# Performance work log

Hardware: AMD Instinct MI355X
Metric: run time of the kernel (lower is better)

The kernel has to match this reference:

```python
import jax, jax.numpy as jnp
import numpy as np
import math

# Model hyperparameters (match init_kwargs)
B, S, E = 8, 1024, 512
NUM_HEADS = 8
NQ = 16        # n_qubits for quantum attention
NQF = 16       # n_qubits_ffn for quantum feed-forward
FFN = 2048
L = 4          # num_layers
EPS = 1e-5


def _sinusoidal_pe(seq_len, embed_dim):
    pos = np.arange(seq_len)[:, None].astype(np.float32)
    div = np.exp(np.arange(0, embed_dim, 2).astype(np.float32) * (-math.log(10000.0) / embed_dim))
    pe = np.zeros((seq_len, embed_dim), dtype=np.float32)
    pe[:, 0::2] = np.sin(pos * div)
    pe[:, 1::2] = np.cos(pos * div)
    return jnp.asarray(pe)


def setup_inputs() -> dict:
    key = jax.random.key(0)
    ks = jax.random.split(key, 12)
    x = jax.random.normal(ks[0], (B, S, E), dtype=jnp.float32)
    pe = _sinusoidal_pe(S, E)
    # per-layer parameters stacked along leading L axis
    theta_attn = jax.random.normal(ks[1], (L, NQ), dtype=jnp.float32) * 0.1   # RY angles (attention circuit)
    theta_ffn = jax.random.normal(ks[2], (L, NQF), dtype=jnp.float32) * 0.1    # RY angles (ffn circuit)
    W_combine = jax.random.normal(ks[3], (L, E, NQ), dtype=jnp.float32) / math.sqrt(NQ)
    W1 = jax.random.normal(ks[4], (L, FFN, NQF), dtype=jnp.float32) / math.sqrt(NQF)
    W2 = jax.random.normal(ks[5], (L, E, FFN), dtype=jnp.float32) / math.sqrt(FFN)
    g1 = jnp.ones((L, E), dtype=jnp.float32)
    b1 = jnp.zeros((L, E), dtype=jnp.float32)
    g2 = jnp.ones((L, E), dtype=jnp.float32)
    b2 = jnp.zeros((L, E), dtype=jnp.float32)
    return {"x": x, "pe": pe, "theta_attn": theta_attn, "theta_ffn": theta_ffn,
            "W_combine": W_combine, "W1": W1, "W2": W2,
            "g1": g1, "b1": b1, "g2": g2, "b2": b2}


def _layer_norm(h, g, b):
    m = jnp.mean(h, axis=-1, keepdims=True)
    v = jnp.var(h, axis=-1, keepdims=True)
    return (h - m) * jax.lax.rsqrt(v + EPS) * g + b


def _quantum_features(h, theta, n_qubits):
    # Each wire: |0> -> RX(x_i) -> RY(theta_i) -> <Z_i> = cos(theta_i) * cos(x_i)
    # Product state => exact closed form; vectorizes the per-token circuit loop.
    return jnp.cos(theta)[None, None, :] * jnp.cos(h[..., :n_qubits])


def reference(x, pe, theta_attn, theta_ffn, W_combine, W1, W2, g1, b1, g2, b2):
    b_, s_, e_ = x.shape
    dk = NQ // NUM_HEADS
    h = x + pe[None, :s_, :]
    for l in range(L):
        qv = _quantum_features(h, theta_attn[l], NQ)                 # [B,S,NQ]
        q = qv.reshape(b_, s_, NUM_HEADS, dk).transpose(0, 2, 1, 3)  # [B,H,S,dk]
        scores = jnp.einsum('bhqd,bhkd->bhqk', q, q) / math.sqrt(dk)
        probs = jax.nn.softmax(scores, axis=-1)
        attn = jnp.einsum('bhqk,bhkd->bhqd', probs, q)               # [B,H,S,dk]
        attn = attn.transpose(0, 2, 1, 3).reshape(b_, s_, NQ)
        attn_out = attn @ W_combine[l].T                             # [B,S,E]
        h = _layer_norm(h + attn_out, g1[l], b1[l])
        # --- quantum feed-forward ---
        qf = _quantum_features(h, theta_ffn[l], NQF)                 # [B,S,NQF]
        ffn_out = jax.nn.relu(qf @ W1[l].T) @ W2[l].T                # [B,S,E]
        h = _layer_norm(h + ffn_out, g2[l], b2[l])
    return h
```

## Files before the change

kernel.cpp:

```cpp
#include <hip/hip_runtime.h>
#include <cstdint>
#include <cstddef>

#define BB 8
#define SS 1024
#define EE 512
#define NQB 16
#define FF 2048

typedef unsigned short u16;
typedef __attribute__((ext_vector_type(8))) short short8;
typedef __attribute__((ext_vector_type(4))) float f32x4;
typedef unsigned int uint_g __attribute__((address_space(1)));
typedef unsigned int uint_l __attribute__((address_space(3)));

#define FLAG_OFF   0
#define H16_OFF    4096
#define QF_OFF     528384
#define W1P_OFF    1052672
#define STATS_OFF  1314816
#define H_OFF      2097152
#define W2P_OFF    18874368

__device__ __forceinline__ float u2f(u16 u){ return __uint_as_float(((unsigned)u)<<16); }
__device__ __forceinline__ u16 f2bf(float x){
  unsigned u = __float_as_uint(x);
  u += 0x7FFF + ((u>>16)&1);
  return (u16)(u>>16);
}
__device__ __forceinline__ float ldg(const void* p,int f,size_t i){
  return f ? ((const float*)p)[i] : u2f(((const u16*)p)[i]);
}
__device__ __forceinline__ float4 ldg4(const void* p,int f,size_t i){
  float4 r;
  if (f){ r = ((const float4*)p)[i>>2]; }
  else { ushort4 v = ((const ushort4*)p)[i>>2];
         r.x=u2f(v.x); r.y=u2f(v.y); r.z=u2f(v.z); r.w=u2f(v.w); }
  return r;
}
__device__ __forceinline__ short8 ldfrag8(const void* p,int f,size_t i){
  short8 r;
  if (f){
    float4 A  = ((const float4*)p)[i>>2];
    float4 Bv = ((const float4*)p)[(i>>2)+1];
    r[0]=(short)f2bf(A.x);  r[1]=(short)f2bf(A.y);  r[2]=(short)f2bf(A.z);  r[3]=(short)f2bf(A.w);
    r[4]=(short)f2bf(Bv.x); r[5]=(short)f2bf(Bv.y); r[6]=(short)f2bf(Bv.z); r[7]=(short)f2bf(Bv.w);
  } else {
    r = *(const short8*)((const u16*)p + i);
  }
  return r;
}
__device__ __forceinline__ void async16(const void* g, void* l){
  __builtin_amdgcn_global_load_lds((const uint_g*)g, (uint_l*)l, 16, 0, 0);
}
__device__ __forceinline__ void tok_stats(const float* st, int tok, float& m, float& rs){
  float S1 = 0.f, S2 = 0.f;
  #pragma unroll
  for (int nb=0; nb<4; ++nb){
    float2 p = *(const float2*)&st[((size_t)tok*4+nb)*2];
    S1 += p.x; S2 += p.y;
  }
  m = S1*(1.f/512.f);
  float var = S2*(1.f/512.f) - m*m;
  rs = rsqrtf(var + 1e-5f);
}

__global__ void detect_k(const u16* __restrict__ x, int* __restrict__ flag){
  __shared__ int cnt;
  if (threadIdx.x==0) cnt=0;
  __syncthreads();
  int c=0;
  for (int i=threadIdx.x;i<4096;i+=256){
    u16 v = x[(size_t)i*2];
    int ex = (v>>7)&0xFF;
    c += (ex>=160) ? 1 : 0;
  }
  atomicAdd(&cnt,c);
  __syncthreads();
  if (threadIdx.x==0) *flag = (cnt>64) ? 1 : 0;
}

__global__ __launch_bounds__(256) void w1pack_k(const void* __restrict__ W1,
    const void* __restrict__ thf, u16* __restrict__ W1p, const int* __restrict__ flag){
  int f = *flag;
  int idx = blockIdx.x*256 + threadIdx.x;
  int l = idx>>12, nt = (idx>>5)&127, lane32 = idx&31;
  int quad = lane32>>4, col = lane32&15;
  short8 v = ldfrag8(W1, f, ((size_t)l*FF + nt*16 + col)*16 + quad*8);
  short8 o;
  #pragma unroll
  for (int j=0;j<8;++j){
    float th = ldg(thf, f, (size_t)l*16 + quad*8 + j);
    o[j] = (short)f2bf(__cosf(th) * u2f((u16)v[j]));
  }
  *(short8*)(W1p + (size_t)idx*8) = o;
}

__global__ __launch_bounds__(256) void w2pack_k(const void* __restrict__ W2,
    u16* __restrict__ W2p, const int* __restrict__ flag){
  int f = *flag;
  int idx = blockIdx.x*256 + threadIdx.x;
  int lane = idx&63, kb = (idx>>6)&63, teg = (idx>>12)&31, l = idx>>17;
  int quad = lane>>4, col = lane&15;
  short8 v = ldfrag8(W2, f, ((size_t)l*EE + teg*16 + col)*FF + kb*32 + quad*8);
  *(short8*)(W2p + (size_t)idx*8) = v;
}

__global__ __launch_bounds__(256) void add_pe_k(const void* __restrict__ x,
    const void* __restrict__ pe, float* __restrict__ hw, const int* __restrict__ flag){
  int f = *flag;
  size_t e = ((size_t)blockIdx.x*256 + threadIdx.x)*4;
  float4 xv = ldg4(x,f,e);
  float4 pv = ldg4(pe,f,e & (size_t)(SS*EE-1));
  float4 o; o.x=xv.x+pv.x; o.y=xv.y+pv.y; o.z=xv.z+pv.z; o.w=xv.w+pv.w;
  *(float4*)&hw[e] = o;
}

__global__ __launch_bounds__(256) void attn_comb_k(float* __restrict__ hw,
    const void* __restrict__ thA, const void* __restrict__ Wc,
    const void* __restrict__ g1v, const void* __restrict__ b1v,
    const void* __restrict__ g2v, const void* __restrict__ b2v,
    const float* __restrict__ st, float* __restrict__ h16,
    float* __restrict__ qf, const int* __restrict__ flag, int lazy, int l){
  __shared__ float SM2[19264];
  float* qq   = SM2;
  float* outC = SM2;
  float* msK  = SM2 + 16640;
  float* AFR  = SM2 + 18688;
  float* MS   = SM2 + 19200;
  float* RS   = SM2 + 19232;
  int f = *flag;
  int tid = threadIdx.x;
  int b = blockIdx.x>>5, grp = blockIdx.x&31;
  size_t bbase = (size_t)b*SS*EE;
  int tok0 = b*SS + grp*32;

  if (lazy){
    #pragma unroll
    for (int t2=0;t2<4;++t2){
      int j = tid*4+t2;
      float m, rs; tok_stats(st, b*SS+j, m, rs);
      msK[j*2]=m; msK[j*2+1]=rs;
    }
  }
  __syncthreads();
  {
    int j0 = tid>>2, d0 = (tid&3)*4;
    float ct[4], gl2[4]={1,1,1,1}, bl2[4]={0,0,0,0};
    #pragma unroll
    for (int d=0;d<4;++d) ct[d] = __cosf(ldg(thA,f,(size_t)l*16+d0+d));
    if (lazy){
      float4 gv = ldg4(g2v,f,(size_t)(l-1)*EE+d0);
      float4 bv = ldg4(b2v,f,(size_t)(l-1)*EE+d0);
      gl2[0]=gv.x; gl2[1]=gv.y; gl2[2]=gv.z; gl2[3]=gv.w;
      bl2[0]=bv.x; bl2[1]=bv.y; bl2[2]=bv.z; bl2[3]=bv.w;
    }
    for (int it=0; it<16; ++it){
      int j = j0 + it*64;
      float4 hv = *(const float4*)&hw[bbase + (size_t)j*EE + d0];
      float vv[4] = {hv.x, hv.y, hv.z, hv.w};
      if (lazy){
        float m = msK[j*2], rs = msK[j*2+1];
        #pragma unroll
        for (int d=0;d<4;++d) vv[d] = fmaf((vv[d]-m)*rs, gl2[d], bl2[d]);
      }
      float4 o;
      o.x = ct[0]*__cosf(vv[0]); o.y = ct[1]*__cosf(vv[1]);
      o.z = ct[2]*__cosf(vv[2]); o.w = ct[3]*__cosf(vv[3]);
      *(float4*)&qq[j*16+d0] = o;
    }
  }
  __syncthreads();
  {
    int r = tid&31, hd = tid>>5;
    int rg = grp*32 + r;
    float a0 = qq[rg*16 + 2*hd], a1 = qq[rg*16 + 2*hd + 1];
    const float sc = 0.70710678118f;
    float a0s = a0*sc, a1s = a1*sc;
    float den=0.f, n0=0.f, n1=0.f;
    for (int j=0;j<SS;++j){
      float2 uv = *(const float2*)&qq[j*16 + 2*hd];
      float e = __expf(fmaf(a1s, uv.y, a0s*uv.x));
      den += e; n0 = fmaf(e, uv.x, n0); n1 = fmaf(e, uv.y, n1);
    }
    float inv = 1.f/den;
    AFR[r*16 + 2*hd] = n0*inv; AFR[r*16 + 2*hd + 1] = n1*inv;
  }
  __syncthreads();
  int e0 = tid*2;
  float wc0[16], wc1[16];
  size_t wb = (size_t)l*EE*16;
  #pragma unroll
  for (int q4=0;q4<4;++q4){
    float4 a = ldg4(Wc,f, wb + (size_t)e0*16     + q4*4);
    float4 bq = ldg4(Wc,f, wb + (size_t)(e0+1)*16 + q4*4);
    wc0[q4*4+0]=a.x; wc0[q4*4+1]=a.y; wc0[q4*4+2]=a.z; wc0[q4*4+3]=a.w;
    wc1[q4*4+0]=bq.x; wc1[q4*4+1]=bq.y; wc1[q4*4+2]=bq.z; wc1[q4*4+3]=bq.w;
  }
  float gl0=1.f,bl0=0.f,gl1=1.f,bl1=0.f;
  if (lazy){
    size_t gb = (size_t)(l-1)*EE;
    gl0 = ldg(g2v,f,gb+e0);   bl0 = ldg(b2v,f,gb+e0);
    gl1 = ldg(g2v,f,gb+e0+1); bl1 = ldg(b2v,f,gb+e0+1);
  }
  for (int t=0; t<32; ++t){
    float2 hr = *(const float2*)&hw[(size_t)(tok0+t)*EE + e0];
    float v0 = hr.x, v1 = hr.y;
    if (lazy){
      float m = msK[(grp*32+t)*2], rs = msK[(grp*32+t)*2+1];
      v0 = fmaf((v0-m)*rs, gl0, bl0);
      v1 = fmaf((v1-m)*rs, gl1, bl1);
    }
    float s0 = v0, s1 = v1;
    #pragma unroll
    for (int q4=0;q4<4;++q4){
      float4 av = *(const float4*)&AFR[t*16 + q4*4];
      s0 = fmaf(av.x, wc0[q4*4+0], fmaf(av.y, wc0[q4*4+1], fmaf(av.z, wc0[q4*4+2], fmaf(av.w, wc0[q4*4+3], s0))));
      s1 = fmaf(av.x, wc1[q4*4+0], fmaf(av.y, wc1[q4*4+1], fmaf(av.z, wc1[q4*4+2], fmaf(av.w, wc1[q4*4+3], s1))));
    }
    outC[t*520 + e0] = s0; outC[t*520 + e0 + 1] = s1;
  }
  __syncthreads();
  {
    int token = tid>>3, prt = tid&7;
    float s=0.f, s2=0.f;
    #pragma unroll 8
    for (int i2=0;i2<64;++i2){
      float vv = outC[token*520 + prt + 8*i2];
      s += vv; s2 = fmaf(vv,vv,s2);
    }
    #pragma unroll
    for (int off=4; off; off>>=1){ s += __shfl_down(s,off,8); s2 += __shfl_down(s2,off,8); }
    if (prt==0){
      float m = s*(1.f/512.f);
      float var = s2*(1.f/512.f) - m*m;
      MS[token] = m; RS[token] = rsqrtf(var+1e-5f);
    }
  }
  __syncthreads();
  for (int u=tid; u<32*128; u+=256){
    int tok = u>>7, c4 = (u&127)*4;
    float4 vv = *(const float4*)&outC[tok*520 + c4];
    float m = MS[tok], rs = RS[tok];
    float4 gv = ldg4(g1v,f,(size_t)l*EE + c4);
    float4 bv = ldg4(b1v,f,(size_t)l*EE + c4);
    float4 o;
    o.x = fmaf((vv.x-m)*rs, gv.x, bv.x);
    o.y = fmaf((vv.y-m)*rs, gv.y, bv.y);
    o.z = fmaf((vv.z-m)*rs, gv.z, bv.z);
    o.w = fmaf((vv.w-m)*rs, gv.w, bv.w);
    if (c4 >= 16){
      *(float4*)&hw[(size_t)(tok0+tok)*EE + c4] = o;
    } else {
      *(float4*)&h16[(size_t)(tok0+tok)*16 + c4] = o;
      float4 qo;
      qo.x=__cosf(o.x); qo.y=__cosf(o.y); qo.z=__cosf(o.z); qo.w=__cosf(o.w);
      *(float4*)&qf[(size_t)(tok0+tok)*16 + c4] = qo;
    }
  }
}

__global__ __launch_bounds__(256) void ffn4_k(float* __restrict__ hw,
    const float* __restrict__ h16, const float* __restrict__ qf,
    const u16* __restrict__ W1p, const void* __restrict__ W2,
    const u16* __restrict__ W2p, float* __restrict__ st,
    const int* __restrict__ flag, int cv, int l){
  __shared__ float SMF[12288];
  u16* W2t = (u16*)SMF;
  u16* HtA = (u16*)SMF + 16384;
  float* outL = SMF;

  int f = *flag;
  int tid = threadIdx.x, w = tid>>6, lane = tid&63;
  int quad = lane>>4, col = lane&15;
  int mb = blockIdx.x, nb = blockIdx.y;
  int tok0 = mb*64;
  int wm = w&1, wn = w>>1;

  short8 a0[4];
  #pragma unroll
  for (int mt=0; mt<4; ++mt){
    short8 z = {0,0,0,0,0,0,0,0};
    if (quad < 2){
      const float* qp = qf + (size_t)(tok0 + mt*16 + col)*16 + quad*8;
      float4 A = *(const float4*)qp, B = *(const float4*)(qp+4);
      z[0]=(short)f2bf(A.x); z[1]=(short)f2bf(A.y); z[2]=(short)f2bf(A.z); z[3]=(short)f2bf(A.w);
      z[4]=(short)f2bf(B.x); z[5]=(short)f2bf(B.y); z[6]=(short)f2bf(B.z); z[7]=(short)f2bf(B.w);
    }
    a0[mt] = z;
  }

  f32x4 acc[2][4];
  #pragma unroll
  for (int i=0;i<2;++i)
    #pragma unroll
    for (int j=0;j<4;++j) acc[i][j] = (f32x4){0.f,0.f,0.f,0.f};
  const f32x4 zc = {0.f,0.f,0.f,0.f};
  size_t w2base = (size_t)l*EE*FF;

  auto stage = [&](int k0, int buf){
    if (cv){
      #pragma unroll
      for (int fi=0; fi<4; ++fi){
        int slot = w*4+fi, te = slot>>1, s = slot&1;
        int kb = (k0>>5) + s;
        const u16* gp = W2p + (((size_t)l*32 + nb*8 + te)*64 + kb)*512 + lane*8;
        async16(gp, &W2t[buf*8192 + slot*512 + lane*8]);
      }
    } else {
      #pragma unroll
      for (int fi=0; fi<4; ++fi){
        int slot = w*4+fi, te = slot>>1, s = slot&1;
        short8 v = ldfrag8(W2, f, w2base + (size_t)(nb*128 + te*16 + col)*FF + k0 + s*32 + quad*8);
        *(short8*)&W2t[buf*8192 + slot*512 + lane*8] = v;
      }
    }
  };
  auto gemm1 = [&](int k0, int buf){
    short8 b1 = {0,0,0,0,0,0,0,0};
    if (quad < 2)
      b1 = *(const short8*)(W1p + (((size_t)l*128 + (k0>>4) + w)*32 + quad*16 + col)*8);
    int kl = w*16 + quad*4;
    int s  = kl>>5, q2 = (kl&31)>>3, j0 = kl&7;
    u16* dst0 = &HtA[buf*4096 + s*512 + (q2*16+col)*8 + j0];
    #pragma unroll
    for (int mt=0; mt<4; ++mt){
      f32x4 hc = __builtin_amdgcn_mfma_f32_16x16x32_bf16(b1, a0[mt], zc, 0,0,0);
      ushort4 pk;
      pk.x = f2bf(fmaxf(hc[0],0.f)); pk.y = f2bf(fmaxf(hc[1],0.f));
      pk.z = f2bf(fmaxf(hc[2],0.f)); pk.w = f2bf(fmaxf(hc[3],0.f));
      *(ushort4*)(dst0 + mt*1024) = pk;
    }
  };

  stage(0, 0); gemm1(0, 0);
  for (int i=0; i<32; ++i){
    __syncthreads();
    int k1 = (i+1)*64;
    if (k1 < FF){ stage(k1, (i+1)&1); gemm1(k1, (i+1)&1); }
    int cb = i&1;
    #pragma unroll
    for (int s=0;s<2;++s){
      short8 A2[2], B2[4];
      A2[0] = *(const short8*)&HtA[cb*4096 + ((wm*2+0)*2+s)*512 + lane*8];
      A2[1] = *(const short8*)&HtA[cb*4096 + ((wm*2+1)*2+s)*512 + lane*8];
      #pragma unroll
      for (int et=0;et<4;++et)
        B2[et] = *(const short8*)&W2t[cb*8192 + ((wn*4+et)*2+s)*512 + lane*8];
      #pragma unroll
      for (int et=0;et<4;++et){
        acc[0][et] = __builtin_amdgcn_mfma_f32_16x16x32_bf16(A2[0], B2[et], acc[0][et], 0,0,0);
        acc[1][et] = __builtin_amdgcn_mfma_f32_16x16x32_bf16(A2[1], B2[et], acc[1][et], 0,0,0);
      }
    }
  }
  __syncthreads();

  #pragma unroll
  for (int mt2=0; mt2<2; ++mt2){
    #pragma unroll
    for (int r=0;r<4;++r){
      int ltok = wm*32 + mt2*16 + quad*4 + r;
      size_t hb = (size_t)(tok0+ltok)*EE + nb*128;
      #pragma unroll
      for (int et=0;et<4;++et){
        int eloc = wn*64 + et*16 + col;
        int eg = nb*128 + eloc;
        float rsd = (eg < 16) ? h16[(size_t)(tok0+ltok)*16 + eg] : hw[hb + eloc];
        outL[ltok*132 + eloc] = acc[mt2][et][r] + rsd;
      }
    }
  }
  __syncthreads();
  {
    int token = tid>>2, prt = tid&3;
    float s=0.f, s2=0.f;
    #pragma unroll 8
    for (int i2=0;i2<32;++i2){
      float vv = outL[token*132 + prt + 4*i2];
      s += vv; s2 = fmaf(vv,vv,s2);
    }
    s += __shfl_down(s,2,4); s2 += __shfl_down(s2,2,4);
    s += __shfl_down(s,1,4); s2 += __shfl_down(s2,1,4);
    if (prt==0){
      float2 o; o.x = s; o.y = s2;
      *(float2*)&st[((size_t)(tok0+token)*4 + nb)*2] = o;
    }
  }
  for (int u=tid; u<64*32; u+=256){
    int tok = u>>5, c4 = (u&31)*4;
    float4 vv = *(const float4*)&outL[tok*132 + c4];
    *(float4*)&hw[(size_t)(tok0+tok)*EE + nb*128 + c4] = vv;
  }
}

__global__ __launch_bounds__(256) void conv2_k(const float* __restrict__ hw,
    const float* __restrict__ st, const void* __restrict__ g2v,
    const void* __restrict__ b2v, void* __restrict__ out,
    const int* __restrict__ flag){
  int f = *flag;
  size_t i = (size_t)blockIdx.x*256 + threadIdx.x;
  int tok = (int)(i>>7), c4 = ((int)i&127)*4;
  float4 v = *(const float4*)&hw[i*4];
  float m, rs; tok_stats(st, tok, m, rs);
  float4 gv = ldg4(g2v,f,(size_t)3*EE + c4);
  float4 bv = ldg4(b2v,f,(size_t)3*EE + c4);
  float4 o;
  o.x = fmaf((v.x-m)*rs, gv.x, bv.x);
  o.y = fmaf((v.y-m)*rs, gv.y, bv.y);
  o.z = fmaf((v.z-m)*rs, gv.z, bv.z);
  o.w = fmaf((v.w-m)*rs, gv.w, bv.w);
  if (f){
    *(float4*)((float*)out + i*4) = o;
  } else {
    ushort4 ob; ob.x=f2bf(o.x); ob.y=f2bf(o.y); ob.z=f2bf(o.z); ob.w=f2bf(o.w);
    *(ushort4*)((u16*)out + i*4) = ob;
  }
}

extern "C" void kernel_launch(void* const* d_in, const int* in_sizes, int n_in,
                              void* d_out, int out_size, void* d_ws, size_t ws_size,
                              hipStream_t stream) {
  (void)in_sizes; (void)n_in; (void)out_size;
  char* ws = (char*)d_ws;
  int*   flag = (int*)(ws + FLAG_OFF);
  float* h16  = (float*)(ws + H16_OFF);
  float* qf   = (float*)(ws + QF_OFF);
  u16*   w1p  = (u16*)(ws + W1P_OFF);
  float* st   = (float*)(ws + STATS_OFF);
  float* hw   = (float*)(ws + H_OFF);
  u16*   w2p  = (u16*)(ws + W2P_OFF);
  int cv = (ws_size >= (size_t)W2P_OFF + ((size_t)8<<20)) ? 1 : 0;

  detect_k<<<1,256,0,stream>>>((const u16*)d_in[0], flag);
  w1pack_k<<<64,256,0,stream>>>(d_in[5], d_in[3], w1p, flag);
  if (cv) w2pack_k<<<2048,256,0,stream>>>(d_in[6], w2p, flag);
  add_pe_k<<<4096,256,0,stream>>>(d_in[0], d_in[1], hw, flag);
  for (int l=0; l<4; ++l){
    int lazy = (l>0) ? 1 : 0;
    attn_comb_k<<<256,256,0,stream>>>(hw, d_in[2], d_in[4], d_in[7], d_in[8],
                                      d_in[9], d_in[10], st, h16, qf,
                                      flag, lazy, l);
    ffn4_k<<<dim3(128,4),256,0,stream>>>(hw, h16, qf, w1p, d_in[6], w2p,
                                         st, flag, cv, l);
  }
  conv2_k<<<4096,256,0,stream>>>(hw, st, d_in[9], d_in[10], d_out, flag);
}
```

Baseline: 448.3 us.

## Split attention key loop across 512 threads and stream W2 directly into registers

The attention/combine kernel now runs 512 threads per block. The softmax key loop is split into two halves whose partial sums are reduced through shared memory, and the q features are stored head-major for float4 reads. The FFN kernel drops LDS staging of W2 and prefetches each wave's W2 fragments straight from global memory into registers. Each wave then owns a 64x32 output tile, which also reduces LDS footprint. This trades LDS traffic and async loads for more register pressure and extra global reads of W2 per block.

```diff
diff --git a/kernel.cpp b/kernel.cpp
--- a/kernel.cpp
+++ b/kernel.cpp
@@ -11,8 +11,6 @@
 typedef unsigned short u16;
 typedef __attribute__((ext_vector_type(8))) short short8;
 typedef __attribute__((ext_vector_type(4))) float f32x4;
-typedef unsigned int uint_g __attribute__((address_space(1)));
-typedef unsigned int uint_l __attribute__((address_space(3)));
 
 #define FLAG_OFF   0
 #define H16_OFF    4096
@@ -50,9 +48,6 @@
   }
   return r;
 }
-__device__ __forceinline__ void async16(const void* g, void* l){
-  __builtin_amdgcn_global_load_lds((const uint_g*)g, (uint_l*)l, 16, 0, 0);
-}
 __device__ __forceinline__ void tok_stats(const float* st, int tok, float& m, float& rs){
   float S1 = 0.f, S2 = 0.f;
   #pragma unroll
@@ -116,19 +111,20 @@
   *(float4*)&hw[e] = o;
 }
 
-__global__ __launch_bounds__(256) void attn_comb_k(float* __restrict__ hw,
+__global__ __launch_bounds__(512) void attn_comb_k(float* __restrict__ hw,
     const void* __restrict__ thA, const void* __restrict__ Wc,
     const void* __restrict__ g1v, const void* __restrict__ b1v,
     const void* __restrict__ g2v, const void* __restrict__ b2v,
     const float* __restrict__ st, float* __restrict__ h16,
     float* __restrict__ qf, const int* __restrict__ flag, int lazy, int l){
-  __shared__ float SM2[19264];
-  float* qq   = SM2;
+  __shared__ float SM2[20544];
+  float* qq2  = SM2;
+  float* part = SM2 + 16384;
+  float* msK  = SM2 + 17920;
+  float* AFR  = SM2 + 19968;
+  float* MS   = SM2 + 20480;
+  float* RS   = SM2 + 20512;
   float* outC = SM2;
-  float* msK  = SM2 + 16640;
-  float* AFR  = SM2 + 18688;
-  float* MS   = SM2 + 19200;
-  float* RS   = SM2 + 19232;
   int f = *flag;
   int tid = threadIdx.x;
   int b = blockIdx.x>>5, grp = blockIdx.x&31;
@@ -137,15 +133,16 @@
 
   if (lazy){
     #pragma unroll
-    for (int t2=0;t2<4;++t2){
-      int j = tid*4+t2;
+    for (int t2=0;t2<2;++t2){
+      int j = tid*2+t2;
       float m, rs; tok_stats(st, b*SS+j, m, rs);
       msK[j*2]=m; msK[j*2+1]=rs;
     }
   }
   __syncthreads();
   {
-    int j0 = tid>>2, d0 = (tid&3)*4;
+    int jl = tid>>2, d0 = (tid&3)*4;
+    int h0 = d0>>1;
     float ct[4], gl2[4]={1,1,1,1}, bl2[4]={0,0,0,0};
     #pragma unroll
     for (int d=0;d<4;++d) ct[d] = __cosf(ldg(thA,f,(size_t)l*16+d0+d));
@@ -155,8 +152,9 @@
       gl2[0]=gv.x; gl2[1]=gv.y; gl2[2]=gv.z; gl2[3]=gv.w;
       bl2[0]=bv.x; bl2[1]=bv.y; bl2[2]=bv.z; bl2[3]=bv.w;
     }
-    for (int it=0; it<16; ++it){
-      int j = j0 + it*64;
+    #pragma unroll 2
+    for (int it=0; it<8; ++it){
+      int j = jl + it*128;
       float4 hv = *(const float4*)&hw[bbase + (size_t)j*EE + d0];
       float vv[4] = {hv.x, hv.y, hv.z, hv.w};
       if (lazy){
@@ -164,73 +162,89 @@
         #pragma unroll
         for (int d=0;d<4;++d) vv[d] = fmaf((vv[d]-m)*rs, gl2[d], bl2[d]);
       }
-      float4 o;
-      o.x = ct[0]*__cosf(vv[0]); o.y = ct[1]*__cosf(vv[1]);
-      o.z = ct[2]*__cosf(vv[2]); o.w = ct[3]*__cosf(vv[3]);
-      *(float4*)&qq[j*16+d0] = o;
-    }
-  }
-  __syncthreads();
-  {
-    int r = tid&31, hd = tid>>5;
+      float2 o0, o1;
+      o0.x = ct[0]*__cosf(vv[0]); o0.y = ct[1]*__cosf(vv[1]);
+      o1.x = ct[2]*__cosf(vv[2]); o1.y = ct[3]*__cosf(vv[3]);
+      *(float2*)&qq2[h0*2048 + j*2]     = o0;
+      *(float2*)&qq2[(h0+1)*2048 + j*2] = o1;
+    }
+  }
+  __syncthreads();
+  {
+    int r = tid&31, hd = (tid>>5)&7, kz = tid>>8;
     int rg = grp*32 + r;
-    float a0 = qq[rg*16 + 2*hd], a1 = qq[rg*16 + 2*hd + 1];
+    const float* qh = &qq2[hd*2048];
+    float a0 = qh[rg*2], a1 = qh[rg*2+1];
     const float sc = 0.70710678118f;
     float a0s = a0*sc, a1s = a1*sc;
-    float den=0.f, n0=0.f, n1=0.f;
-    for (int j=0;j<SS;++j){
-      float2 uv = *(const float2*)&qq[j*16 + 2*hd];
-      float e = __expf(fmaf(a1s, uv.y, a0s*uv.x));
-      den += e; n0 = fmaf(e, uv.x, n0); n1 = fmaf(e, uv.y, n1);
-    }
-    float inv = 1.f/den;
-    AFR[r*16 + 2*hd] = n0*inv; AFR[r*16 + 2*hd + 1] = n1*inv;
-  }
-  __syncthreads();
-  int e0 = tid*2;
-  float wc0[16], wc1[16];
-  size_t wb = (size_t)l*EE*16;
-  #pragma unroll
-  for (int q4=0;q4<4;++q4){
-    float4 a = ldg4(Wc,f, wb + (size_t)e0*16     + q4*4);
-    float4 bq = ldg4(Wc,f, wb + (size_t)(e0+1)*16 + q4*4);
-    wc0[q4*4+0]=a.x; wc0[q4*4+1]=a.y; wc0[q4*4+2]=a.z; wc0[q4*4+3]=a.w;
-    wc1[q4*4+0]=bq.x; wc1[q4*4+1]=bq.y; wc1[q4*4+2]=bq.z; wc1[q4*4+3]=bq.w;
-  }
-  float gl0=1.f,bl0=0.f,gl1=1.f,bl1=0.f;
-  if (lazy){
-    size_t gb = (size_t)(l-1)*EE;
-    gl0 = ldg(g2v,f,gb+e0);   bl0 = ldg(b2v,f,gb+e0);
-    gl1 = ldg(g2v,f,gb+e0+1); bl1 = ldg(b2v,f,gb+e0+1);
-  }
-  for (int t=0; t<32; ++t){
-    float2 hr = *(const float2*)&hw[(size_t)(tok0+t)*EE + e0];
-    float v0 = hr.x, v1 = hr.y;
+    float dA=0.f, x0A=0.f, x1A=0.f, dB=0.f, x0B=0.f, x1B=0.f;
+    const float* qp = qh + kz*1024;
+    for (int j=0; j<512; j+=4){
+      float4 P = *(const float4*)(qp + j*2);
+      float4 Q = *(const float4*)(qp + j*2 + 4);
+      float e0 = __expf(fmaf(a1s,P.y, a0s*P.x));
+      float e1 = __expf(fmaf(a1s,P.w, a0s*P.z));
+      float e2 = __expf(fmaf(a1s,Q.y, a0s*Q.x));
+      float e3 = __expf(fmaf(a1s,Q.w, a0s*Q.z));
+      dA += e0; x0A = fmaf(e0,P.x,x0A); x1A = fmaf(e0,P.y,x1A);
+      dB += e1; x0B = fmaf(e1,P.z,x0B); x1B = fmaf(e1,P.w,x1B);
+      dA += e2; x0A = fmaf(e2,Q.x,x0A); x1A = fmaf(e2,Q.y,x1A);
+      dB += e3; x0B = fmaf(e3,Q.z,x0B); x1B = fmaf(e3,Q.w,x1B);
+    }
+    float* pp = &part[((r*8+hd)*2+kz)*3];
+    pp[0]=dA+dB; pp[1]=x0A+x0B; pp[2]=x1A+x1B;
+  }
+  __syncthreads();
+  if (tid < 256){
+    int r = tid&31, hd = tid>>5;
+    const float* p0 = &part[((r*8+hd)*2+0)*3];
+    const float* p1 = &part[((r*8+hd)*2+1)*3];
+    float d = p0[0]+p1[0];
+    float inv = 1.f/d;
+    AFR[r*16 + 2*hd]   = (p0[1]+p1[1])*inv;
+    AFR[r*16 + 2*hd+1] = (p0[2]+p1[2])*inv;
+  }
+  __syncthreads();
+  {
+    int e0 = tid;
+    float wc[16];
+    size_t wb = (size_t)l*EE*16 + (size_t)e0*16;
+    #pragma unroll
+    for (int q4=0;q4<4;++q4){
+      float4 a = ldg4(Wc,f, wb + q4*4);
+      wc[q4*4+0]=a.x; wc[q4*4+1]=a.y; wc[q4*4+2]=a.z; wc[q4*4+3]=a.w;
+    }
+    float gl0=1.f,bl0=0.f;
     if (lazy){
-      float m = msK[(grp*32+t)*2], rs = msK[(grp*32+t)*2+1];
-      v0 = fmaf((v0-m)*rs, gl0, bl0);
-      v1 = fmaf((v1-m)*rs, gl1, bl1);
-    }
-    float s0 = v0, s1 = v1;
-    #pragma unroll
-    for (int q4=0;q4<4;++q4){
-      float4 av = *(const float4*)&AFR[t*16 + q4*4];
-      s0 = fmaf(av.x, wc0[q4*4+0], fmaf(av.y, wc0[q4*4+1], fmaf(av.z, wc0[q4*4+2], fmaf(av.w, wc0[q4*4+3], s0))));
-      s1 = fmaf(av.x, wc1[q4*4+0], fmaf(av.y, wc1[q4*4+1], fmaf(av.z, wc1[q4*4+2], fmaf(av.w, wc1[q4*4+3], s1))));
-    }
-    outC[t*520 + e0] = s0; outC[t*520 + e0 + 1] = s1;
-  }
-  __syncthreads();
-  {
-    int token = tid>>3, prt = tid&7;
+      gl0 = ldg(g2v,f,(size_t)(l-1)*EE+e0);
+      bl0 = ldg(b2v,f,(size_t)(l-1)*EE+e0);
+    }
+    for (int t=0; t<32; ++t){
+      float v0 = hw[(size_t)(tok0+t)*EE + e0];
+      if (lazy){
+        float m = msK[(grp*32+t)*2], rs = msK[(grp*32+t)*2+1];
+        v0 = fmaf((v0-m)*rs, gl0, bl0);
+      }
+      float s0 = v0;
+      #pragma unroll
+      for (int q4=0;q4<4;++q4){
+        float4 av = *(const float4*)&AFR[t*16 + q4*4];
+        s0 = fmaf(av.x, wc[q4*4+0], fmaf(av.y, wc[q4*4+1], fmaf(av.z, wc[q4*4+2], fmaf(av.w, wc[q4*4+3], s0))));
+      }
+      outC[t*520 + e0] = s0;
+    }
+  }
+  __syncthreads();
+  {
+    int token = tid>>4, prt = tid&15;
     float s=0.f, s2=0.f;
     #pragma unroll 8
-    for (int i2=0;i2<64;++i2){
-      float vv = outC[token*520 + prt + 8*i2];
+    for (int i2=0;i2<32;++i2){
+      float vv = outC[token*520 + prt + 16*i2];
       s += vv; s2 = fmaf(vv,vv,s2);
     }
     #pragma unroll
-    for (int off=4; off; off>>=1){ s += __shfl_down(s,off,8); s2 += __shfl_down(s2,off,8); }
+    for (int off=8; off; off>>=1){ s += __shfl_down(s,off,16); s2 += __shfl_down(s2,off,16); }
     if (prt==0){
       float m = s*(1.f/512.f);
       float var = s2*(1.f/512.f) - m*m;
@@ -238,7 +252,7 @@
     }
   }
   __syncthreads();
-  for (int u=tid; u<32*128; u+=256){
+  for (int u=tid; u<32*128; u+=512){
     int tok = u>>7, c4 = (u&127)*4;
     float4 vv = *(const float4*)&outC[tok*520 + c4];
     float m = MS[tok], rs = RS[tok];
@@ -260,14 +274,13 @@
   }
 }
 
-__global__ __launch_bounds__(256) void ffn4_k(float* __restrict__ hw,
+__global__ __launch_bounds__(256) void ffn5_k(float* __restrict__ hw,
     const float* __restrict__ h16, const float* __restrict__ qf,
     const u16* __restrict__ W1p, const void* __restrict__ W2,
     const u16* __restrict__ W2p, float* __restrict__ st,
     const int* __restrict__ flag, int cv, int l){
-  __shared__ float SMF[12288];
-  u16* W2t = (u16*)SMF;
-  u16* HtA = (u16*)SMF + 16384;
+  __shared__ float SMF[8448];
+  u16* HtA = (u16*)SMF;
   float* outL = SMF;
 
   int f = *flag;
@@ -275,7 +288,6 @@
   int quad = lane>>4, col = lane&15;
   int mb = blockIdx.x, nb = blockIdx.y;
   int tok0 = mb*64;
-  int wm = w&1, wn = w>>1;
 
   short8 a0[4];
   #pragma unroll
@@ -290,36 +302,36 @@
     a0[mt] = z;
   }
 
-  f32x4 acc[2][4];
+  f32x4 acc[4][2];
   #pragma unroll
-  for (int i=0;i<2;++i)
-    #pragma unroll
-    for (int j=0;j<4;++j) acc[i][j] = (f32x4){0.f,0.f,0.f,0.f};
+  for (int i=0;i<4;++i){ acc[i][0]=(f32x4){0,0,0,0}; acc[i][1]=(f32x4){0,0,0,0}; }
   const f32x4 zc = {0.f,0.f,0.f,0.f};
   size_t w2base = (size_t)l*EE*FF;
 
-  auto stage = [&](int k0, int buf){
+  auto loadW1 = [&](int k0)->short8{
+    short8 z = {0,0,0,0,0,0,0,0};
+    if (quad < 2)
+      z = *(const short8*)(W1p + (((size_t)l*128 + (k0>>4) + w)*32 + quad*16 + col)*8);
+    return z;
+  };
+  auto loadB2 = [&](short8 (&B)[2][2], int k0){
     if (cv){
       #pragma unroll
-      for (int fi=0; fi<4; ++fi){
-        int slot = w*4+fi, te = slot>>1, s = slot&1;
-        int kb = (k0>>5) + s;
-        const u16* gp = W2p + (((size_t)l*32 + nb*8 + te)*64 + kb)*512 + lane*8;
-        async16(gp, &W2t[buf*8192 + slot*512 + lane*8]);
-      }
+      for (int et=0;et<2;++et)
+        #pragma unroll
+        for (int s=0;s<2;++s)
+          B[et][s] = *(const short8*)(W2p + ((((size_t)l*32 + nb*8 + w*2 + et)*64)
+                       + (k0>>5) + s)*512 + lane*8);
     } else {
       #pragma unroll
-      for (int fi=0; fi<4; ++fi){
-        int slot = w*4+fi, te = slot>>1, s = slot&1;
-        short8 v = ldfrag8(W2, f, w2base + (size_t)(nb*128 + te*16 + col)*FF + k0 + s*32 + quad*8);
-        *(short8*)&W2t[buf*8192 + slot*512 + lane*8] = v;
-      }
+      for (int et=0;et<2;++et)
+        #pragma unroll
+        for (int s=0;s<2;++s)
+          B[et][s] = ldfrag8(W2, f, w2base
+                       + (size_t)(nb*128 + w*32 + et*16 + col)*FF + k0 + s*32 + quad*8);
     }
   };
-  auto gemm1 = [&](int k0, int buf){
-    short8 b1 = {0,0,0,0,0,0,0,0};
-    if (quad < 2)
-      b1 = *(const short8*)(W1p + (((size_t)l*128 + (k0>>4) + w)*32 + quad*16 + col)*8);
+  auto gemm1 = [&](int buf, short8 b1){
     int kl = w*16 + quad*4;
     int s  = kl>>5, q2 = (kl&31)>>3, j0 = kl&7;
     u16* dst0 = &HtA[buf*4096 + s*512 + (q2*16+col)*8 + j0];
@@ -333,41 +345,54 @@
     }
   };
 
-  stage(0, 0); gemm1(0, 0);
+  short8 B2c[2][2], B2n[2][2];
+  short8 b1n;
+  {
+    short8 b1 = loadW1(0);
+    loadB2(B2c, 0);
+    gemm1(0, b1);
+    b1n = loadW1(64);
+  }
+  __syncthreads();
   for (int i=0; i<32; ++i){
+    if (i < 31){
+      loadB2(B2n, (i+1)*64);
+      gemm1((i+1)&1, b1n);
+      int k2 = (i+2 < 32) ? (i+2)*64 : 0;
+      b1n = loadW1(k2);
+    }
+    int cb = i&1;
+    #pragma unroll
+    for (int s=0;s<2;++s){
+      short8 A2[4];
+      #pragma unroll
+      for (int mt=0;mt<4;++mt)
+        A2[mt] = *(const short8*)&HtA[cb*4096 + (mt*2+s)*512 + lane*8];
+      #pragma unroll
+      for (int et=0;et<2;++et)
+        #pragma unroll
+        for (int mt=0;mt<4;++mt)
+          acc[mt][et] = __builtin_amdgcn_mfma_f32_16x16x32_bf16(A2[mt], B2c[et][s], acc[mt][et], 0,0,0);
+    }
     __syncthreads();
-    int k1 = (i+1)*64;
-    if (k1 < FF){ stage(k1, (i+1)&1); gemm1(k1, (i+1)&1); }
-    int cb = i&1;
-    #pragma unroll
-    for (int s=0;s<2;++s){
-      short8 A2[2], B2[4];
-      A2[0] = *(const short8*)&HtA[cb*4096 + ((wm*2+0)*2+s)*512 + lane*8];
-      A2[1] = *(const short8*)&HtA[cb*4096 + ((wm*2+1)*2+s)*512 + lane*8];
-      #pragma unroll
-      for (int et=0;et<4;++et)
-        B2[et] = *(const short8*)&W2t[cb*8192 + ((wn*4+et)*2+s)*512 + lane*8];
-      #pragma unroll
-      for (int et=0;et<4;++et){
-        acc[0][et] = __builtin_amdgcn_mfma_f32_16x16x32_bf16(A2[0], B2[et], acc[0][et], 0,0,0);
-        acc[1][et] = __builtin_amdgcn_mfma_f32_16x16x32_bf16(A2[1], B2[et], acc[1][et], 0,0,0);
-      }
-    }
-  }
-  __syncthreads();
+    if (i < 31){
+      #pragma unroll
+      for (int et=0;et<2;++et){ B2c[et][0]=B2n[et][0]; B2c[et][1]=B2n[et][1]; }
+    }
+  }
 
   #pragma unroll
-  for (int mt2=0; mt2<2; ++mt2){
+  for (int mt=0; mt<4; ++mt){
     #pragma unroll
     for (int r=0;r<4;++r){
-      int ltok = wm*32 + mt2*16 + quad*4 + r;
+      int ltok = mt*16 + quad*4 + r;
       size_t hb = (size_t)(tok0+ltok)*EE + nb*128;
       #pragma unroll
-      for (int et=0;et<4;++et){
-        int eloc = wn*64 + et*16 + col;
+      for (int et=0;et<2;++et){
+        int eloc = w*32 + et*16 + col;
         int eg = nb*128 + eloc;
         float rsd = (eg < 16) ? h16[(size_t)(tok0+ltok)*16 + eg] : hw[hb + eloc];
-        outL[ltok*132 + eloc] = acc[mt2][et][r] + rsd;
+        outL[ltok*132 + eloc] = acc[mt][et][r] + rsd;
       }
     }
   }
@@ -438,10 +463,10 @@
   add_pe_k<<<4096,256,0,stream>>>(d_in[0], d_in[1], hw, flag);
   for (int l=0; l<4; ++l){
     int lazy = (l>0) ? 1 : 0;
-    attn_comb_k<<<256,256,0,stream>>>(hw, d_in[2], d_in[4], d_in[7], d_in[8],
+    attn_comb_k<<<256,512,0,stream>>>(hw, d_in[2], d_in[4], d_in[7], d_in[8],
                                       d_in[9], d_in[10], st, h16, qf,
                                       flag, lazy, l);
-    ffn4_k<<<dim3(128,4),256,0,stream>>>(hw, h16, qf, w1p, d_in[6], w2p,
+    ffn5_k<<<dim3(128,4),256,0,stream>>>(hw, h16, qf, w1p, d_in[6], w2p,
                                          st, flag, cv, l);
   }
   conv2_k<<<4096,256,0,stream>>>(hw, st, d_in[9], d_in[10], d_out, flag);
```

Measured after the change: 399.6 us. -10.9%, faster.
